# Kernel optimization log

Hardware: AMD Instinct MI355X
Metric: run time of the kernel (lower is better)

The kernel has to match this reference:

```python
import jax, jax.numpy as jnp
import numpy as np

EPS = 1e-5  # torch nn.LayerNorm default eps
N_SUBJECTS = 16


def _gelu(x):
    # torch nn.GELU default = exact erf formulation
    return jax.nn.gelu(x, approximate=False)


def setup_inputs() -> dict:
    key = jax.random.key(0)
    ks = jax.random.split(key, 8)
    B, D = 131072, 512
    x = jax.random.normal(ks[0], (B, D), dtype=jnp.float32)
    groups = jax.random.randint(ks[1], (B,), 0, N_SUBJECTS, dtype=jnp.int32)
    # LayerNorm affine params: rows 0..15 subject-specific, row 16 = default_norm
    gammas = jnp.ones((N_SUBJECTS + 1, D), dtype=jnp.float32)
    betas = jnp.zeros((N_SUBJECTS + 1, D), dtype=jnp.float32)
    # Domain classifier MLP (xavier-uniform weights, zero biases)
    def xavier(k, fan_in, fan_out):
        lim = np.sqrt(6.0 / (fan_in + fan_out)).astype(np.float32)
        return jax.random.uniform(k, (fan_in, fan_out), dtype=jnp.float32,
                                  minval=-lim, maxval=lim)
    W1 = xavier(ks[2], D, 256); b1 = jnp.zeros((256,), jnp.float32)
    W2 = xavier(ks[3], 256, 128); b2 = jnp.zeros((128,), jnp.float32)
    W3 = xavier(ks[4], 128, N_SUBJECTS); b3 = jnp.zeros((N_SUBJECTS,), jnp.float32)
    return {"x": x, "groups": groups, "gammas": gammas, "betas": betas,
            "W1": W1, "b1": b1, "W2": W2, "b2": b2, "W3": W3, "b3": b3}


def _subject_layernorm(x, groups, gammas, betas):
    # Fused per-row LayerNorm with per-subject affine params.
    # Out-of-range subject ids (>= N_SUBJECTS or < 0) use the default row (index N_SUBJECTS).
    valid = (groups >= 0) & (groups < N_SUBJECTS)
    idx = jnp.where(valid, groups, N_SUBJECTS)
    g = gammas[idx]  # (B, D)
    b = betas[idx]   # (B, D)
    mu = jnp.mean(x, axis=-1, keepdims=True)
    var = jnp.mean(jnp.square(x - mu), axis=-1, keepdims=True)  # biased, as torch LN
    xn = (x - mu) * jax.lax.rsqrt(var + EPS)
    return xn * g + b


def _domain_classifier(x, W1, b1, W2, b2, W3, b3):
    # Dropout is identity in eval mode
    h = _gelu(x @ W1 + b1)
    h = _gelu(h @ W2 + b2)
    return h @ W3 + b3


def reference(x, groups, gammas, betas, W1, b1, W2, b2, W3, b3):
    # gradient reversal is identity in forward
    domain_logits = _domain_classifier(x, W1, b1, W2, b2, W3, b3)
    normalized_x = _subject_layernorm(x, groups, gammas, betas)
    return (normalized_x, domain_logits)
```

## Files before the change

kernel.cpp:

```cpp
#include <hip/hip_runtime.h>
#include <hip/hip_bf16.h>
#include <stdint.h>

#define NSUB 16

typedef short  bf16x8 __attribute__((ext_vector_type(8)));
typedef float  f32x4  __attribute__((ext_vector_type(4)));
typedef unsigned int u32x4 __attribute__((ext_vector_type(4)));

__device__ __forceinline__ float gelu_exact(float x){
  return 0.5f * x * (1.0f + erff(x * 0.70710678118654752440f));
}

__device__ __forceinline__ float gelu_fast(float x){
  float xx = x * x;
  float m  = fmaf(0.044715f, xx, 1.0f);
  float a  = x * m * -2.3022084f;
  float e  = __builtin_amdgcn_exp2f(a);
  float r  = __builtin_amdgcn_rcpf(e + 1.0f);
  return x * r;
}

__device__ __forceinline__ unsigned short f2bf(float f){
  union { float f; uint32_t u; } v; v.f = f;
  uint32_t u = v.u;
  return (unsigned short)((u + 0x7FFFu + ((u >> 16) & 1u)) >> 16);
}

__device__ __forceinline__ unsigned int pk2(float lo, float hi){
  union { __hip_bfloat162 b; unsigned int u; } c;
  c.b = __float22bfloat162_rn(make_float2(lo, hi));
  return c.u;
}

__device__ __forceinline__ bf16x8 as_bf(u32x4 v){
  union { u32x4 u; bf16x8 b; } c; c.u = v; return c.b;
}

__device__ __forceinline__ float bflo(unsigned int u){
  union { unsigned int u; float f; } c; c.u = u << 16; return c.f;
}
__device__ __forceinline__ float bfhi(unsigned int u){
  union { unsigned int u; float f; } c; c.u = u & 0xffff0000u; return c.f;
}

__global__ __launch_bounds__(256) void wconv_kernel(
    const float* __restrict__ W1, const float* __restrict__ W2, const float* __restrict__ W3,
    unsigned short* __restrict__ W1f, unsigned short* __restrict__ W2f, unsigned short* __restrict__ W3f){
  int t = blockIdx.x * 256 + threadIdx.x;
  if (t < 131072){
    int n = t >> 9, k = t & 511;
    int lane = ((k >> 3) & 3) * 16 + (n & 15);
    int idx = (((k >> 5) * 16 + (n >> 4)) * 64 + lane) * 8 + (k & 7);
    W1f[idx] = f2bf(W1[k*256 + n]);
  } else if (t < 163840){
    int i = t - 131072; int n = i >> 8, k = i & 255;
    int lane = ((k >> 3) & 3) * 16 + (n & 15);
    int idx = (((k >> 5) * 8 + (n >> 4)) * 64 + lane) * 8 + (k & 7);
    W2f[idx] = f2bf(W2[k*128 + n]);
  } else if (t < 165888){
    int i = t - 163840; int n = i >> 7, k = i & 127;
    int lane = ((k >> 3) & 3) * 16 + n;
    int idx = ((k >> 5) * 64 + lane) * 8 + (k & 7);
    W3f[idx] = f2bf(W3[k*16 + n]);
  }
}

__global__ __launch_bounds__(512, 8) void fused_kernel(
    const float* __restrict__ x, const int* __restrict__ groups,
    const float* __restrict__ gammas, const float* __restrict__ betas,
    const unsigned short* __restrict__ W1f, const float* __restrict__ b1,
    const unsigned short* __restrict__ W2f, const float* __restrict__ b2,
    const unsigned short* __restrict__ W3f, const float* __restrict__ b3,
    float* __restrict__ ln_out, float* __restrict__ out2){
  __shared__ __align__(16) uint8_t smem[32768];
  constexpr int OFF_H2 = 16384;

  const int tid  = threadIdx.x;
  const int wave = tid >> 6;
  const int lane = tid & 63;
  const int l15  = lane & 15;
  const int g4   = lane >> 4;
  const int row0 = blockIdx.x * 32;

  const int sr  = tid >> 4;
  const int sc  = tid & 15;
  const int swz = (sr & 7) << 4;
  uint8_t* xrow = smem + sr*1024;
  const float* xg = x + (size_t)(row0 + sr)*512 + sc*8;

  int gi   = groups[row0 + sr];
  int gidx = ((unsigned)gi < (unsigned)NSUB) ? gi : NSUB;

  float s = 0.f, q = 0.f;
  #pragma unroll
  for (int c = 0; c < 4; ++c){
    f32x4 v0 = *(const f32x4*)(xg + c*128);
    f32x4 v1 = *(const f32x4*)(xg + c*128 + 4);
    s += v0.x + v0.y + v0.z + v0.w + v1.x + v1.y + v1.z + v1.w;
    q += v0.x*v0.x + v0.y*v0.y + v0.z*v0.z + v0.w*v0.w
       + v1.x*v1.x + v1.y*v1.y + v1.z*v1.z + v1.w*v1.w;
    u32x4 pw;
    pw.x = pk2(v0.x, v0.y); pw.y = pk2(v0.z, v0.w);
    pw.z = pk2(v1.x, v1.y); pw.w = pk2(v1.z, v1.w);
    *(u32x4*)(xrow + ((c*256 + sc*16) ^ swz)) = pw;
  }
  s += __shfl_xor(s, 1); s += __shfl_xor(s, 2);
  s += __shfl_xor(s, 4); s += __shfl_xor(s, 8);
  q += __shfl_xor(q, 1); q += __shfl_xor(q, 2);
  q += __shfl_xor(q, 4); q += __shfl_xor(q, 8);
  float mu  = s * (1.0f/512.0f);
  float var = q * (1.0f/512.0f) - mu*mu;
  float rs  = rsqrtf(var + 1e-5f);
  float nmr = -mu * rs;

  u32x4 braw[4][2];
  #pragma unroll
  for (int p = 0; p < 3; ++p)
    #pragma unroll
    for (int n = 0; n < 2; ++n)
      braw[p][n] = *(const u32x4*)(W1f + (size_t)(((p*16 + wave*2 + n)*64 + lane)*8));

  float b1v[2];
  #pragma unroll
  for (int n = 0; n < 2; ++n) b1v[n] = b1[wave*32 + n*16 + l15];
  float b2v = b2[wave*16 + l15];
  float b3v = b3[l15];

  {
    const float* gpr = gammas + (size_t)gidx*512 + sc*8;
    const float* bpr = betas  + (size_t)gidx*512 + sc*8;
    float* op = ln_out + (size_t)(row0 + sr)*512 + sc*8;
    #pragma unroll
    for (int c = 0; c < 4; ++c){
      u32x4 pw = *(const u32x4*)(xrow + ((c*256 + sc*16) ^ swz));
      f32x4 g0 = *(const f32x4*)(gpr + c*128);
      f32x4 g1 = *(const f32x4*)(gpr + c*128 + 4);
      f32x4 e0 = *(const f32x4*)(bpr + c*128);
      f32x4 e1 = *(const f32x4*)(bpr + c*128 + 4);
      f32x4 o0, o1;
      o0.x = fmaf(fmaf(bflo(pw.x), rs, nmr), g0.x, e0.x);
      o0.y = fmaf(fmaf(bfhi(pw.x), rs, nmr), g0.y, e0.y);
      o0.z = fmaf(fmaf(bflo(pw.y), rs, nmr), g0.z, e0.z);
      o0.w = fmaf(fmaf(bfhi(pw.y), rs, nmr), g0.w, e0.w);
      o1.x = fmaf(fmaf(bflo(pw.z), rs, nmr), g1.x, e1.x);
      o1.y = fmaf(fmaf(bfhi(pw.z), rs, nmr), g1.y, e1.y);
      o1.z = fmaf(fmaf(bflo(pw.w), rs, nmr), g1.z, e1.z);
      o1.w = fmaf(fmaf(bfhi(pw.w), rs, nmr), g1.w, e1.w);
      *(f32x4*)(op + c*128)     = o0;
      *(f32x4*)(op + c*128 + 4) = o1;
    }
  }

  int baseA[2][2];
  #pragma unroll
  for (int m = 0; m < 2; ++m){
    int row = m*16 + l15;
    int sw  = (row & 7) << 4;
    int bse = row*1024 + ((g4*16) ^ (sw & 0x30));
    int kx  = (row >> 2) & 1;
    baseA[m][0] = bse + ((0 ^ kx) << 6);
    baseA[m][1] = bse + ((1 ^ kx) << 6);
  }

  __syncthreads();

  f32x4 acc1[2][2] = {};
  #pragma unroll
  for (int g = 0; g < 16; ++g){
    if (g < 13){
      #pragma unroll
      for (int n = 0; n < 2; ++n)
        braw[(g+3)&3][n] = *(const u32x4*)(W1f + (size_t)((((g+3)*16 + wave*2 + n)*64 + lane)*8));
    }
    bf16x8 a[2];
    #pragma unroll
    for (int m = 0; m < 2; ++m)
      a[m] = *(const bf16x8*)(smem + baseA[m][g & 1] + (g >> 1)*128);
    #pragma unroll
    for (int m = 0; m < 2; ++m)
      #pragma unroll
      for (int n = 0; n < 2; ++n)
        acc1[m][n] = __builtin_amdgcn_mfma_f32_16x16x32_bf16(a[m], as_bf(braw[g & 3][n]), acc1[m][n], 0, 0, 0);
  }

  u32x4 b2raw[4];
  #pragma unroll
  for (int p = 0; p < 3; ++p)
    b2raw[p] = *(const u32x4*)(W2f + (size_t)(((p*8 + wave)*64 + lane)*8));

  __syncthreads();

  #pragma unroll
  for (int n = 0; n < 2; ++n){
    #pragma unroll
    for (int m = 0; m < 2; ++m){
      #pragma unroll
      for (int r = 0; r < 4; ++r){
        int row = m*16 + g4*4 + r;
        int col = wave*32 + n*16 + l15;
        float v = gelu_fast(acc1[m][n][r] + b1v[n]);
        *(unsigned short*)(smem + row*512 + ((col*2) ^ ((row & 7) << 4))) = f2bf(v);
      }
    }
  }
  __syncthreads();

  int baseH[2][2];
  #pragma unroll
  for (int m = 0; m < 2; ++m){
    int row = m*16 + l15;
    int sw  = (row & 7) << 4;
    int bse = row*512 + ((g4*16) ^ (sw & 0x30));
    int kx  = (row >> 2) & 1;
    baseH[m][0] = bse + ((0 ^ kx) << 6);
    baseH[m][1] = bse + ((1 ^ kx) << 6);
  }
  f32x4 acc2[2] = {};
  #pragma unroll
  for (int g = 0; g < 8; ++g){
    if (g < 5)
      b2raw[(g+3)&3] = *(const u32x4*)(W2f + (size_t)((((g+3)*8 + wave)*64 + lane)*8));
    bf16x8 a[2];
    #pragma unroll
    for (int m = 0; m < 2; ++m)
      a[m] = *(const bf16x8*)(smem + baseH[m][g & 1] + (g >> 1)*128);
    #pragma unroll
    for (int m = 0; m < 2; ++m)
      acc2[m] = __builtin_amdgcn_mfma_f32_16x16x32_bf16(a[m], as_bf(b2raw[g & 3]), acc2[m], 0, 0, 0);
  }

  u32x4 b3raw[4];
  #pragma unroll
  for (int ks = 0; ks < 4; ++ks)
    b3raw[ks] = *(const u32x4*)(W3f + (size_t)((ks*64 + lane)*8));

  #pragma unroll
  for (int m = 0; m < 2; ++m){
    #pragma unroll
    for (int r = 0; r < 4; ++r){
      int row = m*16 + g4*4 + r;
      int col = wave*16 + l15;
      float v = gelu_fast(acc2[m][r] + b2v);
      *(unsigned short*)(smem + OFF_H2 + row*256 + ((col*2) ^ ((row & 7) << 4))) = f2bf(v);
    }
  }
  __syncthreads();

  if (wave < 2){
    int baseG[2];
    {
      int row = wave*16 + l15;
      int sw  = (row & 7) << 4;
      int bse = OFF_H2 + row*256 + ((g4*16) ^ (sw & 0x30));
      int kx  = (row >> 2) & 1;
      baseG[0] = bse + ((0 ^ kx) << 6);
      baseG[1] = bse + ((1 ^ kx) << 6);
    }
    f32x4 acc3 = {};
    #pragma unroll
    for (int ks = 0; ks < 4; ++ks){
      bf16x8 a = *(const bf16x8*)(smem + baseG[ks & 1] + (ks >> 1)*128);
      acc3 = __builtin_amdgcn_mfma_f32_16x16x32_bf16(a, as_bf(b3raw[ks]), acc3, 0, 0, 0);
    }
    #pragma unroll
    for (int r = 0; r < 4; ++r){
      int grow = row0 + wave*16 + g4*4 + r;
      out2[(size_t)grow*16 + l15] = acc3[r] + b3v;
    }
  }
}

__global__ __launch_bounds__(256) void ln_kernel(
    const float* __restrict__ x, const int* __restrict__ groups,
    const float* __restrict__ gammas, const float* __restrict__ betas,
    float* __restrict__ out){
  int row  = blockIdx.x * 4 + (threadIdx.x >> 6);
  int lane = threadIdx.x & 63;
  const float4* xr = (const float4*)(x + (size_t)row * 512);
  float4 a = xr[lane];
  float4 b = xr[lane + 64];
  float s = a.x + a.y + a.z + a.w + b.x + b.y + b.z + b.w;
  float q = a.x*a.x + a.y*a.y + a.z*a.z + a.w*a.w
          + b.x*b.x + b.y*b.y + b.z*b.z + b.w*b.w;
  #pragma unroll
  for (int o = 32; o > 0; o >>= 1){
    s += __shfl_xor(s, o);
    q += __shfl_xor(q, o);
  }
  float mu  = s * (1.0f/512.0f);
  float var = q * (1.0f/512.0f) - mu*mu;
  float rsq = rsqrtf(var + 1e-5f);
  int gi = groups[row];
  int idx = ((unsigned)gi < (unsigned)NSUB) ? gi : NSUB;
  const float4* gr = (const float4*)(gammas + (size_t)idx * 512);
  const float4* br = (const float4*)(betas  + (size_t)idx * 512);
  float4 g0 = gr[lane], g1 = gr[lane + 64];
  float4 e0 = br[lane], e1 = br[lane + 64];
  float4 o0, o1;
  o0.x = (a.x - mu)*rsq*g0.x + e0.x; o0.y = (a.y - mu)*rsq*g0.y + e0.y;
  o0.z = (a.z - mu)*rsq*g0.z + e0.z; o0.w = (a.w - mu)*rsq*g0.w + e0.w;
  o1.x = (b.x - mu)*rsq*g1.x + e1.x; o1.y = (b.y - mu)*rsq*g1.y + e1.y;
  o1.z = (b.z - mu)*rsq*g1.z + e1.z; o1.w = (b.w - mu)*rsq*g1.w + e1.w;
  float4* orow = (float4*)(out + (size_t)row * 512);
  orow[lane]      = o0;
  orow[lane + 64] = o1;
}

__global__ __launch_bounds__(256) void mlp_naive(
    const float* __restrict__ x,
    const float* __restrict__ W1, const float* __restrict__ b1,
    const float* __restrict__ W2, const float* __restrict__ b2,
    const float* __restrict__ W3, const float* __restrict__ b3,
    float* __restrict__ out2){
  __shared__ float xr[512];
  __shared__ float h1[256];
  __shared__ float h2[128];
  int row = blockIdx.x, t = threadIdx.x;
  xr[t]       = x[(size_t)row*512 + t];
  xr[t + 256] = x[(size_t)row*512 + t + 256];
  __syncthreads();
  {
    float s = 0.f;
    for (int k = 0; k < 512; ++k) s += xr[k] * W1[k*256 + t];
    h1[t] = gelu_exact(s + b1[t]);
  }
  __syncthreads();
  if (t < 128){
    float s = 0.f;
    for (int k = 0; k < 256; ++k) s += h1[k] * W2[k*128 + t];
    h2[t] = gelu_exact(s + b2[t]);
  }
  __syncthreads();
  if (t < 16){
    float s = 0.f;
    for (int k = 0; k < 128; ++k) s += h2[k] * W3[k*16 + t];
    out2[(size_t)row*16 + t] = s + b3[t];
  }
}

extern "C" void kernel_launch(void* const* d_in, const int* in_sizes, int n_in,
                              void* d_out, int out_size, void* d_ws, size_t ws_size,
                              hipStream_t stream){
  const float* x      = (const float*)d_in[0];
  const int*   groups = (const int*)d_in[1];
  const float* gammas = (const float*)d_in[2];
  const float* betas  = (const float*)d_in[3];
  const float* W1 = (const float*)d_in[4];
  const float* b1 = (const float*)d_in[5];
  const float* W2 = (const float*)d_in[6];
  const float* b2 = (const float*)d_in[7];
  const float* W3 = (const float*)d_in[8];
  const float* b3 = (const float*)d_in[9];
  float* out  = (float*)d_out;
  const int B = in_sizes[0] / 512;
  float* out2 = out + (size_t)B * 512;

  const int n_u16 = 131072 + 32768 + 2048;
  const size_t ws_need = (size_t)n_u16 * sizeof(unsigned short);
  if (ws_size >= ws_need){
    unsigned short* W1f = (unsigned short*)d_ws;
    unsigned short* W2f = W1f + 131072;
    unsigned short* W3f = W2f + 32768;
    wconv_kernel<<<(n_u16 + 255)/256, 256, 0, stream>>>(W1, W2, W3, W1f, W2f, W3f);
    fused_kernel<<<B/32, 512, 0, stream>>>(x, groups, gammas, betas,
                                           W1f, b1, W2f, b2, W3f, b3, out, out2);
  } else {
    mlp_naive<<<B, 256, 0, stream>>>(x, W1, b1, W2, b2, W3, b3, out2);
    ln_kernel<<<B/4, 256, 0, stream>>>(x, groups, gammas, betas, out);
  }
}
```

Baseline: 170.9 us.

## Double block to 64 rows and 16 waves, remapping MFMA work per wave

The fused LayerNorm+MLP kernel now processes 64 rows per block with 1024 threads and 64KB of LDS instead of 32 rows with 512 threads. In layer 1 each wave computes a single 16-column slice across all 4 row tiles, so each W1 fragment is reused across more rows. Layers 2 and 3 are split across the two row halves. The weight prefetch depth drops from 3 stages to 1 to cut register use. Weight traffic per row falls, in exchange for fewer resident blocks per CU and less latency hiding on the global weight loads.

```diff
diff --git a/kernel.cpp b/kernel.cpp
--- a/kernel.cpp
+++ b/kernel.cpp
@@ -66,22 +66,22 @@
   }
 }
 
-__global__ __launch_bounds__(512, 8) void fused_kernel(
+__global__ __launch_bounds__(1024, 4) void fused_kernel(
     const float* __restrict__ x, const int* __restrict__ groups,
     const float* __restrict__ gammas, const float* __restrict__ betas,
     const unsigned short* __restrict__ W1f, const float* __restrict__ b1,
     const unsigned short* __restrict__ W2f, const float* __restrict__ b2,
     const unsigned short* __restrict__ W3f, const float* __restrict__ b3,
     float* __restrict__ ln_out, float* __restrict__ out2){
-  __shared__ __align__(16) uint8_t smem[32768];
-  constexpr int OFF_H2 = 16384;
+  __shared__ __align__(16) uint8_t smem[65536];
+  constexpr int OFF_H2 = 32768;
 
   const int tid  = threadIdx.x;
   const int wave = tid >> 6;
   const int lane = tid & 63;
   const int l15  = lane & 15;
   const int g4   = lane >> 4;
-  const int row0 = blockIdx.x * 32;
+  const int row0 = blockIdx.x * 64;
 
   const int sr  = tid >> 4;
   const int sc  = tid & 15;
@@ -94,16 +94,16 @@
 
   float s = 0.f, q = 0.f;
   #pragma unroll
-  for (int c = 0; c < 4; ++c){
-    f32x4 v0 = *(const f32x4*)(xg + c*128);
-    f32x4 v1 = *(const f32x4*)(xg + c*128 + 4);
+  for (int t = 0; t < 4; ++t){
+    f32x4 v0 = *(const f32x4*)(xg + t*128);
+    f32x4 v1 = *(const f32x4*)(xg + t*128 + 4);
     s += v0.x + v0.y + v0.z + v0.w + v1.x + v1.y + v1.z + v1.w;
     q += v0.x*v0.x + v0.y*v0.y + v0.z*v0.z + v0.w*v0.w
        + v1.x*v1.x + v1.y*v1.y + v1.z*v1.z + v1.w*v1.w;
     u32x4 pw;
     pw.x = pk2(v0.x, v0.y); pw.y = pk2(v0.z, v0.w);
     pw.z = pk2(v1.x, v1.y); pw.w = pk2(v1.z, v1.w);
-    *(u32x4*)(xrow + ((c*256 + sc*16) ^ swz)) = pw;
+    *(u32x4*)(xrow + ((t*256 + sc*16) ^ swz)) = pw;
   }
   s += __shfl_xor(s, 1); s += __shfl_xor(s, 2);
   s += __shfl_xor(s, 4); s += __shfl_xor(s, 8);
@@ -114,17 +114,11 @@
   float rs  = rsqrtf(var + 1e-5f);
   float nmr = -mu * rs;
 
-  u32x4 braw[4][2];
-  #pragma unroll
-  for (int p = 0; p < 3; ++p)
-    #pragma unroll
-    for (int n = 0; n < 2; ++n)
-      braw[p][n] = *(const u32x4*)(W1f + (size_t)(((p*16 + wave*2 + n)*64 + lane)*8));
-
-  float b1v[2];
-  #pragma unroll
-  for (int n = 0; n < 2; ++n) b1v[n] = b1[wave*32 + n*16 + l15];
-  float b2v = b2[wave*16 + l15];
+  u32x4 braw[2];
+  braw[0] = *(const u32x4*)(W1f + (size_t)((wave*64 + lane)*8));
+
+  float b1v = b1[wave*16 + l15];
+  float b2v = b2[(wave & 7)*16 + l15];
   float b3v = b3[l15];
 
   {
@@ -132,12 +126,12 @@
     const float* bpr = betas  + (size_t)gidx*512 + sc*8;
     float* op = ln_out + (size_t)(row0 + sr)*512 + sc*8;
     #pragma unroll
-    for (int c = 0; c < 4; ++c){
-      u32x4 pw = *(const u32x4*)(xrow + ((c*256 + sc*16) ^ swz));
-      f32x4 g0 = *(const f32x4*)(gpr + c*128);
-      f32x4 g1 = *(const f32x4*)(gpr + c*128 + 4);
-      f32x4 e0 = *(const f32x4*)(bpr + c*128);
-      f32x4 e1 = *(const f32x4*)(bpr + c*128 + 4);
+    for (int t = 0; t < 4; ++t){
+      u32x4 pw = *(const u32x4*)(xrow + ((t*256 + sc*16) ^ swz));
+      f32x4 g0 = *(const f32x4*)(gpr + t*128);
+      f32x4 g1 = *(const f32x4*)(gpr + t*128 + 4);
+      f32x4 e0 = *(const f32x4*)(bpr + t*128);
+      f32x4 e1 = *(const f32x4*)(bpr + t*128 + 4);
       f32x4 o0, o1;
       o0.x = fmaf(fmaf(bflo(pw.x), rs, nmr), g0.x, e0.x);
       o0.y = fmaf(fmaf(bfhi(pw.x), rs, nmr), g0.y, e0.y);
@@ -147,14 +141,14 @@
       o1.y = fmaf(fmaf(bfhi(pw.z), rs, nmr), g1.y, e1.y);
       o1.z = fmaf(fmaf(bflo(pw.w), rs, nmr), g1.z, e1.z);
       o1.w = fmaf(fmaf(bfhi(pw.w), rs, nmr), g1.w, e1.w);
-      *(f32x4*)(op + c*128)     = o0;
-      *(f32x4*)(op + c*128 + 4) = o1;
-    }
-  }
-
-  int baseA[2][2];
-  #pragma unroll
-  for (int m = 0; m < 2; ++m){
+      *(f32x4*)(op + t*128)     = o0;
+      *(f32x4*)(op + t*128 + 4) = o1;
+    }
+  }
+
+  int baseA[4][2];
+  #pragma unroll
+  for (int m = 0; m < 4; ++m){
     int row = m*16 + l15;
     int sw  = (row & 7) << 4;
     int bse = row*1024 + ((g4*16) ^ (sw & 0x30));
@@ -165,51 +159,45 @@
 
   __syncthreads();
 
-  f32x4 acc1[2][2] = {};
+  f32x4 acc1[4] = {};
   #pragma unroll
   for (int g = 0; g < 16; ++g){
-    if (g < 13){
-      #pragma unroll
-      for (int n = 0; n < 2; ++n)
-        braw[(g+3)&3][n] = *(const u32x4*)(W1f + (size_t)((((g+3)*16 + wave*2 + n)*64 + lane)*8));
-    }
-    bf16x8 a[2];
-    #pragma unroll
-    for (int m = 0; m < 2; ++m)
+    if (g < 15)
+      braw[(g+1)&1] = *(const u32x4*)(W1f + (size_t)((((g+1)*16 + wave)*64 + lane)*8));
+    bf16x8 a[4];
+    #pragma unroll
+    for (int m = 0; m < 4; ++m)
       a[m] = *(const bf16x8*)(smem + baseA[m][g & 1] + (g >> 1)*128);
     #pragma unroll
-    for (int m = 0; m < 2; ++m)
-      #pragma unroll
-      for (int n = 0; n < 2; ++n)
-        acc1[m][n] = __builtin_amdgcn_mfma_f32_16x16x32_bf16(a[m], as_bf(braw[g & 3][n]), acc1[m][n], 0, 0, 0);
-  }
-
-  u32x4 b2raw[4];
-  #pragma unroll
-  for (int p = 0; p < 3; ++p)
-    b2raw[p] = *(const u32x4*)(W2f + (size_t)(((p*8 + wave)*64 + lane)*8));
-
-  __syncthreads();
-
-  #pragma unroll
-  for (int n = 0; n < 2; ++n){
-    #pragma unroll
-    for (int m = 0; m < 2; ++m){
+    for (int m = 0; m < 4; ++m)
+      acc1[m] = __builtin_amdgcn_mfma_f32_16x16x32_bf16(a[m], as_bf(braw[g & 1]), acc1[m], 0, 0, 0);
+  }
+
+  u32x4 b2raw[2];
+  b2raw[0] = *(const u32x4*)(W2f + (size_t)(((wave & 7)*64 + lane)*8));
+
+  __syncthreads();
+
+  {
+    int col = wave*16 + l15;
+    #pragma unroll
+    for (int m = 0; m < 4; ++m){
       #pragma unroll
       for (int r = 0; r < 4; ++r){
         int row = m*16 + g4*4 + r;
-        int col = wave*32 + n*16 + l15;
-        float v = gelu_fast(acc1[m][n][r] + b1v[n]);
+        float v = gelu_fast(acc1[m][r] + b1v);
         *(unsigned short*)(smem + row*512 + ((col*2) ^ ((row & 7) << 4))) = f2bf(v);
       }
     }
   }
   __syncthreads();
 
+  const int mh  = wave >> 3;
+  const int nn2 = wave & 7;
   int baseH[2][2];
   #pragma unroll
   for (int m = 0; m < 2; ++m){
-    int row = m*16 + l15;
+    int row = (mh*2 + m)*16 + l15;
     int sw  = (row & 7) << 4;
     int bse = row*512 + ((g4*16) ^ (sw & 0x30));
     int kx  = (row >> 2) & 1;
@@ -219,35 +207,39 @@
   f32x4 acc2[2] = {};
   #pragma unroll
   for (int g = 0; g < 8; ++g){
-    if (g < 5)
-      b2raw[(g+3)&3] = *(const u32x4*)(W2f + (size_t)((((g+3)*8 + wave)*64 + lane)*8));
+    if (g < 7)
+      b2raw[(g+1)&1] = *(const u32x4*)(W2f + (size_t)((((g+1)*8 + nn2)*64 + lane)*8));
     bf16x8 a[2];
     #pragma unroll
     for (int m = 0; m < 2; ++m)
       a[m] = *(const bf16x8*)(smem + baseH[m][g & 1] + (g >> 1)*128);
     #pragma unroll
     for (int m = 0; m < 2; ++m)
-      acc2[m] = __builtin_amdgcn_mfma_f32_16x16x32_bf16(a[m], as_bf(b2raw[g & 3]), acc2[m], 0, 0, 0);
+      acc2[m] = __builtin_amdgcn_mfma_f32_16x16x32_bf16(a[m], as_bf(b2raw[g & 1]), acc2[m], 0, 0, 0);
   }
 
   u32x4 b3raw[4];
-  #pragma unroll
-  for (int ks = 0; ks < 4; ++ks)
-    b3raw[ks] = *(const u32x4*)(W3f + (size_t)((ks*64 + lane)*8));
-
-  #pragma unroll
-  for (int m = 0; m < 2; ++m){
-    #pragma unroll
-    for (int r = 0; r < 4; ++r){
-      int row = m*16 + g4*4 + r;
-      int col = wave*16 + l15;
-      float v = gelu_fast(acc2[m][r] + b2v);
-      *(unsigned short*)(smem + OFF_H2 + row*256 + ((col*2) ^ ((row & 7) << 4))) = f2bf(v);
-    }
-  }
-  __syncthreads();
-
-  if (wave < 2){
+  if (wave < 4){
+    #pragma unroll
+    for (int ks = 0; ks < 4; ++ks)
+      b3raw[ks] = *(const u32x4*)(W3f + (size_t)((ks*64 + lane)*8));
+  }
+
+  {
+    int col = nn2*16 + l15;
+    #pragma unroll
+    for (int m = 0; m < 2; ++m){
+      #pragma unroll
+      for (int r = 0; r < 4; ++r){
+        int row = (mh*2 + m)*16 + g4*4 + r;
+        float v = gelu_fast(acc2[m][r] + b2v);
+        *(unsigned short*)(smem + OFF_H2 + row*256 + ((col*2) ^ ((row & 7) << 4))) = f2bf(v);
+      }
+    }
+  }
+  __syncthreads();
+
+  if (wave < 4){
     int baseG[2];
     {
       int row = wave*16 + l15;
@@ -277,9 +269,9 @@
     float* __restrict__ out){
   int row  = blockIdx.x * 4 + (threadIdx.x >> 6);
   int lane = threadIdx.x & 63;
-  const float4* xr = (const float4*)(x + (size_t)row * 512);
-  float4 a = xr[lane];
-  float4 b = xr[lane + 64];
+  const float4* xrp = (const float4*)(x + (size_t)row * 512);
+  float4 a = xrp[lane];
+  float4 b = xrp[lane + 64];
   float s = a.x + a.y + a.z + a.w + b.x + b.y + b.z + b.w;
   float q = a.x*a.x + a.y*a.y + a.z*a.z + a.w*a.w
           + b.x*b.x + b.y*b.y + b.z*b.z + b.w*b.w;
@@ -363,8 +355,8 @@
     unsigned short* W2f = W1f + 131072;
     unsigned short* W3f = W2f + 32768;
     wconv_kernel<<<(n_u16 + 255)/256, 256, 0, stream>>>(W1, W2, W3, W1f, W2f, W3f);
-    fused_kernel<<<B/32, 512, 0, stream>>>(x, groups, gammas, betas,
-                                           W1f, b1, W2f, b2, W3f, b3, out, out2);
+    fused_kernel<<<B/64, 1024, 0, stream>>>(x, groups, gammas, betas,
+                                            W1f, b1, W2f, b2, W3f, b3, out, out2);
   } else {
     mlp_naive<<<B, 256, 0, stream>>>(x, W1, b1, W2, b2, W3, b3, out2);
     ln_kernel<<<B/4, 256, 0, stream>>>(x, groups, gammas, betas, out);
```

Result: slower. 177.4 us (+3.8%).

## Split fused kernel into separate LayerNorm and MLP blocks by block parity

Applied to the files above, without the earlier changes.

Launches twice as many blocks. Odd blocks do the LayerNorm for their 32 rows straight from fp32 global x, reading x twice. Even blocks only convert x to bf16 in shared memory and run the MLP. This removes the bf16 round-trip in the LayerNorm output and lets LN work run alongside the MFMA blocks, but it doubles global reads of x. It also lowers the launch-bounds occupancy hint from 8 to 4, which may change register allocation.

```diff
diff --git a/kernel.cpp b/kernel.cpp
--- a/kernel.cpp
+++ b/kernel.cpp
@@ -35,13 +35,6 @@
 
 __device__ __forceinline__ bf16x8 as_bf(u32x4 v){
   union { u32x4 u; bf16x8 b; } c; c.u = v; return c.b;
-}
-
-__device__ __forceinline__ float bflo(unsigned int u){
-  union { unsigned int u; float f; } c; c.u = u << 16; return c.f;
-}
-__device__ __forceinline__ float bfhi(unsigned int u){
-  union { unsigned int u; float f; } c; c.u = u & 0xffff0000u; return c.f;
 }
 
 __global__ __launch_bounds__(256) void wconv_kernel(
@@ -66,7 +59,7 @@
   }
 }
 
-__global__ __launch_bounds__(512, 8) void fused_kernel(
+__global__ __launch_bounds__(512, 4) void fused_kernel(
     const float* __restrict__ x, const int* __restrict__ groups,
     const float* __restrict__ gammas, const float* __restrict__ betas,
     const unsigned short* __restrict__ W1f, const float* __restrict__ b1,
@@ -77,80 +70,91 @@
   constexpr int OFF_H2 = 16384;
 
   const int tid  = threadIdx.x;
-  const int wave = tid >> 6;
-  const int lane = tid & 63;
-  const int l15  = lane & 15;
-  const int g4   = lane >> 4;
-  const int row0 = blockIdx.x * 32;
-
-  const int sr  = tid >> 4;
-  const int sc  = tid & 15;
-  const int swz = (sr & 7) << 4;
-  uint8_t* xrow = smem + sr*1024;
-  const float* xg = x + (size_t)(row0 + sr)*512 + sc*8;
-
-  int gi   = groups[row0 + sr];
-  int gidx = ((unsigned)gi < (unsigned)NSUB) ? gi : NSUB;
-
-  float s = 0.f, q = 0.f;
-  #pragma unroll
-  for (int c = 0; c < 4; ++c){
-    f32x4 v0 = *(const f32x4*)(xg + c*128);
-    f32x4 v1 = *(const f32x4*)(xg + c*128 + 4);
-    s += v0.x + v0.y + v0.z + v0.w + v1.x + v1.y + v1.z + v1.w;
-    q += v0.x*v0.x + v0.y*v0.y + v0.z*v0.z + v0.w*v0.w
-       + v1.x*v1.x + v1.y*v1.y + v1.z*v1.z + v1.w*v1.w;
-    u32x4 pw;
-    pw.x = pk2(v0.x, v0.y); pw.y = pk2(v0.z, v0.w);
-    pw.z = pk2(v1.x, v1.y); pw.w = pk2(v1.z, v1.w);
-    *(u32x4*)(xrow + ((c*256 + sc*16) ^ swz)) = pw;
-  }
-  s += __shfl_xor(s, 1); s += __shfl_xor(s, 2);
-  s += __shfl_xor(s, 4); s += __shfl_xor(s, 8);
-  q += __shfl_xor(q, 1); q += __shfl_xor(q, 2);
-  q += __shfl_xor(q, 4); q += __shfl_xor(q, 8);
-  float mu  = s * (1.0f/512.0f);
-  float var = q * (1.0f/512.0f) - mu*mu;
-  float rs  = rsqrtf(var + 1e-5f);
-  float nmr = -mu * rs;
-
-  u32x4 braw[4][2];
-  #pragma unroll
-  for (int p = 0; p < 3; ++p)
-    #pragma unroll
-    for (int n = 0; n < 2; ++n)
-      braw[p][n] = *(const u32x4*)(W1f + (size_t)(((p*16 + wave*2 + n)*64 + lane)*8));
-
-  float b1v[2];
-  #pragma unroll
-  for (int n = 0; n < 2; ++n) b1v[n] = b1[wave*32 + n*16 + l15];
-  float b2v = b2[wave*16 + l15];
-  float b3v = b3[l15];
-
-  {
+  const int row0 = (blockIdx.x >> 1) * 32;
+
+  if (blockIdx.x & 1){
+    const int sr = tid >> 4;
+    const int sc = tid & 15;
+    const float* xg = x + (size_t)(row0 + sr)*512 + sc*8;
+    float s = 0.f, q = 0.f;
+    #pragma unroll
+    for (int c = 0; c < 4; ++c){
+      f32x4 v0 = *(const f32x4*)(xg + c*128);
+      f32x4 v1 = *(const f32x4*)(xg + c*128 + 4);
+      s += v0.x + v0.y + v0.z + v0.w + v1.x + v1.y + v1.z + v1.w;
+      q += v0.x*v0.x + v0.y*v0.y + v0.z*v0.z + v0.w*v0.w
+         + v1.x*v1.x + v1.y*v1.y + v1.z*v1.z + v1.w*v1.w;
+    }
+    s += __shfl_xor(s, 1); s += __shfl_xor(s, 2);
+    s += __shfl_xor(s, 4); s += __shfl_xor(s, 8);
+    q += __shfl_xor(q, 1); q += __shfl_xor(q, 2);
+    q += __shfl_xor(q, 4); q += __shfl_xor(q, 8);
+    float mu  = s * (1.0f/512.0f);
+    float var = q * (1.0f/512.0f) - mu*mu;
+    float rs  = rsqrtf(var + 1e-5f);
+    float nmr = -mu * rs;
+    int gi   = groups[row0 + sr];
+    int gidx = ((unsigned)gi < (unsigned)NSUB) ? gi : NSUB;
     const float* gpr = gammas + (size_t)gidx*512 + sc*8;
     const float* bpr = betas  + (size_t)gidx*512 + sc*8;
     float* op = ln_out + (size_t)(row0 + sr)*512 + sc*8;
     #pragma unroll
     for (int c = 0; c < 4; ++c){
-      u32x4 pw = *(const u32x4*)(xrow + ((c*256 + sc*16) ^ swz));
+      f32x4 v0 = *(const f32x4*)(xg + c*128);
+      f32x4 v1 = *(const f32x4*)(xg + c*128 + 4);
       f32x4 g0 = *(const f32x4*)(gpr + c*128);
       f32x4 g1 = *(const f32x4*)(gpr + c*128 + 4);
       f32x4 e0 = *(const f32x4*)(bpr + c*128);
       f32x4 e1 = *(const f32x4*)(bpr + c*128 + 4);
       f32x4 o0, o1;
-      o0.x = fmaf(fmaf(bflo(pw.x), rs, nmr), g0.x, e0.x);
-      o0.y = fmaf(fmaf(bfhi(pw.x), rs, nmr), g0.y, e0.y);
-      o0.z = fmaf(fmaf(bflo(pw.y), rs, nmr), g0.z, e0.z);
-      o0.w = fmaf(fmaf(bfhi(pw.y), rs, nmr), g0.w, e0.w);
-      o1.x = fmaf(fmaf(bflo(pw.z), rs, nmr), g1.x, e1.x);
-      o1.y = fmaf(fmaf(bfhi(pw.z), rs, nmr), g1.y, e1.y);
-      o1.z = fmaf(fmaf(bflo(pw.w), rs, nmr), g1.z, e1.z);
-      o1.w = fmaf(fmaf(bfhi(pw.w), rs, nmr), g1.w, e1.w);
+      o0.x = fmaf(fmaf(v0.x, rs, nmr), g0.x, e0.x);
+      o0.y = fmaf(fmaf(v0.y, rs, nmr), g0.y, e0.y);
+      o0.z = fmaf(fmaf(v0.z, rs, nmr), g0.z, e0.z);
+      o0.w = fmaf(fmaf(v0.w, rs, nmr), g0.w, e0.w);
+      o1.x = fmaf(fmaf(v1.x, rs, nmr), g1.x, e1.x);
+      o1.y = fmaf(fmaf(v1.y, rs, nmr), g1.y, e1.y);
+      o1.z = fmaf(fmaf(v1.z, rs, nmr), g1.z, e1.z);
+      o1.w = fmaf(fmaf(v1.w, rs, nmr), g1.w, e1.w);
       *(f32x4*)(op + c*128)     = o0;
       *(f32x4*)(op + c*128 + 4) = o1;
     }
-  }
+    return;
+  }
+
+  const int wave = tid >> 6;
+  const int lane = tid & 63;
+  const int l15  = lane & 15;
+  const int g4   = lane >> 4;
+
+  {
+    const int sr  = tid >> 4;
+    const int sc  = tid & 15;
+    const int swz = (sr & 7) << 4;
+    uint8_t* xrow = smem + sr*1024;
+    const float* xg = x + (size_t)(row0 + sr)*512 + sc*8;
+    #pragma unroll
+    for (int c = 0; c < 4; ++c){
+      f32x4 v0 = *(const f32x4*)(xg + c*128);
+      f32x4 v1 = *(const f32x4*)(xg + c*128 + 4);
+      u32x4 pw;
+      pw.x = pk2(v0.x, v0.y); pw.y = pk2(v0.z, v0.w);
+      pw.z = pk2(v1.x, v1.y); pw.w = pk2(v1.z, v1.w);
+      *(u32x4*)(xrow + ((c*256 + sc*16) ^ swz)) = pw;
+    }
+  }
+
+  u32x4 braw[4][2];
+  #pragma unroll
+  for (int p = 0; p < 3; ++p)
+    #pragma unroll
+    for (int n = 0; n < 2; ++n)
+      braw[p][n] = *(const u32x4*)(W1f + (size_t)(((p*16 + wave*2 + n)*64 + lane)*8));
+
+  float b1v[2];
+  #pragma unroll
+  for (int n = 0; n < 2; ++n) b1v[n] = b1[wave*32 + n*16 + l15];
+  float b2v = b2[wave*16 + l15];
+  float b3v = b3[l15];
 
   int baseA[2][2];
   #pragma unroll
@@ -277,9 +281,9 @@
     float* __restrict__ out){
   int row  = blockIdx.x * 4 + (threadIdx.x >> 6);
   int lane = threadIdx.x & 63;
-  const float4* xr = (const float4*)(x + (size_t)row * 512);
-  float4 a = xr[lane];
-  float4 b = xr[lane + 64];
+  const float4* xrp = (const float4*)(x + (size_t)row * 512);
+  float4 a = xrp[lane];
+  float4 b = xrp[lane + 64];
   float s = a.x + a.y + a.z + a.w + b.x + b.y + b.z + b.w;
   float q = a.x*a.x + a.y*a.y + a.z*a.z + a.w*a.w
           + b.x*b.x + b.y*b.y + b.z*b.z + b.w*b.w;
@@ -363,8 +367,8 @@
     unsigned short* W2f = W1f + 131072;
     unsigned short* W3f = W2f + 32768;
     wconv_kernel<<<(n_u16 + 255)/256, 256, 0, stream>>>(W1, W2, W3, W1f, W2f, W3f);
-    fused_kernel<<<B/32, 512, 0, stream>>>(x, groups, gammas, betas,
-                                           W1f, b1, W2f, b2, W3f, b3, out, out2);
+    fused_kernel<<<2*(B/32), 512, 0, stream>>>(x, groups, gammas, betas,
+                                               W1f, b1, W2f, b2, W3f, b3, out, out2);
   } else {
     mlp_naive<<<B, 256, 0, stream>>>(x, W1, b1, W2, b2, W3, b3, out2);
     ln_kernel<<<B/4, 256, 0, stream>>>(x, groups, gammas, betas, out);
```

Result: slower. 185.3 us (+8.4%).
